# Kernel tuning notes

Measured on AMD Instinct MI355X. Metric: run time of the kernel, lower is better.

## Reference

```python
import jax, jax.numpy as jnp
import numpy as np

N_NODES = 100000
N_EDGES = 3200000
D_IN = 128
D_OUT = 128


def setup_inputs() -> dict:
    key = jax.random.key(0)
    k1, k2, k3, k4, k5, k6 = jax.random.split(key, 6)
    x = jax.random.normal(k1, (N_NODES, D_IN), dtype=jnp.float32)
    weight = jax.random.normal(k2, (D_OUT, D_IN), dtype=jnp.float32)
    bias = jax.random.normal(k3, (D_OUT,), dtype=jnp.float32)
    edge_vals = jax.random.uniform(k4, (N_EDGES,), dtype=jnp.float32)
    edge_rows = jax.random.randint(k5, (N_EDGES,), 0, N_NODES, dtype=jnp.int32)
    edge_cols = jax.random.randint(k6, (N_EDGES,), 0, N_NODES, dtype=jnp.int32)
    return {"x": x, "weight": weight, "bias": bias,
            "edge_vals": edge_vals, "edge_rows": edge_rows, "edge_cols": edge_cols}


def reference(x, weight, bias, edge_vals, edge_rows, edge_cols):
    # h = Linear(x): [N, D_OUT]
    h = jnp.einsum('ni,oi->no', x, weight) + bias
    # out = A @ h with A in COO form: out[r] += v * h[c]
    msgs = edge_vals[:, None] * h[edge_cols]  # [E, D_OUT]
    out = jax.ops.segment_sum(msgs, edge_rows, num_segments=N_NODES)
    return out
```

## Files before the change

### kernel.cpp

```cpp
#include <hip/hip_runtime.h>
#include <hip/hip_bf16.h>

#define D 128
#define RPB 256
#define RPB_SHIFT 8
#define NBMAX 512
#define P1CHUNK 8192
#define CAP 9216
#define OVFCAP 4096

using bf16x8 = __attribute__((ext_vector_type(8))) short;
using f32x4  = __attribute__((ext_vector_type(4))) float;
using f32x2  = __attribute__((ext_vector_type(2))) float;

static __device__ inline unsigned short f2bf(float f) {
    __hip_bfloat16 b = __float2bfloat16(f);
    return reinterpret_cast<unsigned short&>(b);
}

__global__ __launch_bounds__(256) void gemm_mfma_kernel(
    const float* __restrict__ x, const float* __restrict__ W,
    const float* __restrict__ bias, __hip_bfloat16* __restrict__ h, int N)
{
    __shared__ unsigned short sA[128 * 128];
    __shared__ unsigned short sB[128 * 128];

    const int tid   = threadIdx.x;
    const int nbase = blockIdx.x * 128;

#pragma unroll
    for (int it = 0; it < 16; ++it) {
        const int r = it * 8 + (tid >> 5);
        const int c = (tid & 31) * 4;
        const unsigned addr = (unsigned)((r * 256 + c * 2) ^ ((r & 7) << 4));

        const int gr = nbase + r;
        float4 xv = make_float4(0.f, 0.f, 0.f, 0.f);
        if (gr < N) xv = *reinterpret_cast<const float4*>(x + (size_t)gr * D + c);
        ushort4 xb = make_ushort4(f2bf(xv.x), f2bf(xv.y), f2bf(xv.z), f2bf(xv.w));
        *reinterpret_cast<ushort4*>(reinterpret_cast<char*>(sA) + addr) = xb;

        float4 wv = *reinterpret_cast<const float4*>(W + (size_t)r * D + c);
        ushort4 wb = make_ushort4(f2bf(wv.x), f2bf(wv.y), f2bf(wv.z), f2bf(wv.w));
        *reinterpret_cast<ushort4*>(reinterpret_cast<char*>(sB) + addr) = wb;
    }
    __syncthreads();

    const int wid  = tid >> 6;
    const int lane = tid & 63;
    const int wr   = (wid >> 1) * 64;
    const int wc   = (wid & 1) * 64;
    const int lrow = lane & 15;
    const int lkb  = (lane >> 4) * 16;

    f32x4 acc[4][4] = {};

#pragma unroll
    for (int kk = 0; kk < 4; ++kk) {
        const int kbyte = kk * 64 + lkb;
        bf16x8 a[4], b[4];
#pragma unroll
        for (int m = 0; m < 4; ++m) {
            const int row = wr + m * 16 + lrow;
            const unsigned addr = (unsigned)((row * 256 + kbyte) ^ ((row & 7) << 4));
            a[m] = *reinterpret_cast<const bf16x8*>(reinterpret_cast<const char*>(sA) + addr);
        }
#pragma unroll
        for (int n = 0; n < 4; ++n) {
            const int row = wc + n * 16 + lrow;
            const unsigned addr = (unsigned)((row * 256 + kbyte) ^ ((row & 7) << 4));
            b[n] = *reinterpret_cast<const bf16x8*>(reinterpret_cast<const char*>(sB) + addr);
        }
#pragma unroll
        for (int m = 0; m < 4; ++m)
#pragma unroll
            for (int n = 0; n < 4; ++n)
                acc[m][n] = __builtin_amdgcn_mfma_f32_16x16x32_bf16(a[m], b[n], acc[m][n], 0, 0, 0);
    }

    float bv[4];
#pragma unroll
    for (int n = 0; n < 4; ++n) bv[n] = bias[wc + n * 16 + lrow];

#pragma unroll
    for (int m = 0; m < 4; ++m) {
        const int row0 = nbase + wr + m * 16 + (lane >> 4) * 4;
#pragma unroll
        for (int n = 0; n < 4; ++n) {
            const int col = wc + n * 16 + lrow;
#pragma unroll
            for (int r = 0; r < 4; ++r) {
                const int grow = row0 + r;
                if (grow < N)
                    h[(size_t)grow * D + col] = __float2bfloat16(acc[m][n][r] + bv[n]);
            }
        }
    }
}

__global__ __launch_bounds__(256) void pass1_fixed_kernel(
    const int* __restrict__ rows, const int* __restrict__ cols,
    const float* __restrict__ vals,
    int* __restrict__ bcount,
    uint2* __restrict__ pairs,
    uint4* __restrict__ ovf,
    int NB, int E)
{
    __shared__ int srows[P1CHUNK];
    __shared__ int lh[NBMAX];
    __shared__ int lbase[NBMAX];

    const int tid  = threadIdx.x;
    const int base = blockIdx.x * P1CHUNK;

    for (int i = tid; i < NBMAX; i += 256) lh[i] = 0;
    __syncthreads();

#pragma unroll 4
    for (int it = 0; it < P1CHUNK / 256; ++it) {
        int e = base + it * 256 + tid;
        int r = (e < E) ? rows[e] : -1;
        srows[it * 256 + tid] = r;
        if (r >= 0) atomicAdd(&lh[r >> RPB_SHIFT], 1);
    }
    __syncthreads();

    for (int i = tid; i < NBMAX; i += 256) {
        int c = lh[i];
        lbase[i] = c ? (i * CAP + atomicAdd(&bcount[i], c)) : 0;
        lh[i] = 0;
    }
    __syncthreads();

#pragma unroll 4
    for (int it = 0; it < P1CHUNK / 256; ++it) {
        int e = base + it * 256 + tid;
        int r = srows[it * 256 + tid];
        if (r < 0) continue;
        int b = r >> RPB_SHIFT;
        int lofs = atomicAdd(&lh[b], 1);
        int pos = lbase[b] + lofs;
        if (pos < (b + 1) * CAP) {
            unsigned packed = ((unsigned)(r & (RPB - 1)) << 17) | (unsigned)cols[e];
            pairs[pos] = make_uint2(packed, __float_as_uint(vals[e]));
        } else {
            int oi = atomicAdd(&bcount[NB], 1);
            if (oi < OVFCAP)
                ovf[oi] = make_uint4((unsigned)r, (unsigned)cols[e],
                                     __float_as_uint(vals[e]), 0u);
        }
    }
}

__global__ __launch_bounds__(256) void pass2_fixed_kernel(
    uint2* __restrict__ pairs, const int* __restrict__ bcount,
    int* __restrict__ rowstart, int* __restrict__ rowend, int N)
{
    __shared__ uint2 st[CAP];
    __shared__ int rh[RPB];
    __shared__ int sc[RPB];
    __shared__ int cur[RPB];

    const int b   = blockIdx.x;
    const int tid = threadIdx.x;
    const int start = b * CAP;
    int cnt = bcount[b];
    if (cnt > CAP) cnt = CAP;

    rh[tid] = 0;
    __syncthreads();

    for (int i = tid; i < cnt; i += 256) {
        uint2 p = pairs[start + i];
        st[i] = p;
        atomicAdd(&rh[p.x >> 17], 1);
    }
    __syncthreads();

    int myc = rh[tid];
    sc[tid] = myc;
    __syncthreads();
    for (int off = 1; off < 256; off <<= 1) {
        int t = (tid >= off) ? sc[tid - off] : 0;
        __syncthreads();
        sc[tid] += t;
        __syncthreads();
    }
    int excl = sc[tid] - myc;
    cur[tid] = start + excl;
    int grow = b * RPB + tid;
    if (grow < N) {
        rowstart[grow] = start + excl;
        rowend[grow]   = start + excl + myc;
    }
    __syncthreads();

    for (int i = tid; i < cnt; i += 256) {
        uint2 p = st[i];
        int r = (int)(p.x >> 17);
        int pos = atomicAdd(&cur[r], 1);
        pairs[pos] = make_uint2(p.x & 0x1FFFFu, p.y);
    }
}

__global__ __launch_bounds__(256) void row_gather2_kernel(
    const __hip_bfloat16* __restrict__ hbf, const uint2* __restrict__ pairs,
    const int* __restrict__ rowstart, const int* __restrict__ rowend,
    float* __restrict__ out, int N)
{
    int row  = (int)((blockIdx.x * (size_t)blockDim.x + threadIdx.x) >> 6);
    int lane = threadIdx.x & 63;
    if (row >= N) return;

    int start = rowstart[row];
    int end   = rowend[row];

    const char* hb = reinterpret_cast<const char*>(hbf);
    const unsigned lbyte = (unsigned)lane << 2;
    float ax = 0.f, ay = 0.f;

    for (int e0 = start; e0 < end; e0 += 64) {
        int pl = e0 + lane;
        if (pl >= end) pl = end - 1;
        uint2 p = pairs[pl];
        int pc = (int)p.x, pv = (int)p.y;
        int m = end - e0; if (m > 64) m = 64;

        int idx = 0;
        const int m16 = m & ~15;
        for (; idx < m16; idx += 16) {
            unsigned c[16], vb[16], hv[16];
#pragma unroll
            for (int u = 0; u < 16; ++u) {
                c[u]  = (unsigned)__builtin_amdgcn_readlane(pc, idx + u);
                vb[u] = (unsigned)__builtin_amdgcn_readlane(pv, idx + u);
            }
#pragma unroll
            for (int u = 0; u < 16; ++u)
                hv[u] = *reinterpret_cast<const unsigned*>(hb + (((size_t)c[u]) << 8) + lbyte);
#pragma unroll
            for (int u = 0; u < 16; ++u) {
                float v = __uint_as_float(vb[u]);
                ax += v * __uint_as_float(hv[u] << 16);
                ay += v * __uint_as_float(hv[u] & 0xffff0000u);
            }
        }
        const int m8 = m & ~7;
        for (; idx < m8; idx += 8) {
            unsigned c[8], vb[8], hv[8];
#pragma unroll
            for (int u = 0; u < 8; ++u) {
                c[u]  = (unsigned)__builtin_amdgcn_readlane(pc, idx + u);
                vb[u] = (unsigned)__builtin_amdgcn_readlane(pv, idx + u);
            }
#pragma unroll
            for (int u = 0; u < 8; ++u)
                hv[u] = *reinterpret_cast<const unsigned*>(hb + (((size_t)c[u]) << 8) + lbyte);
#pragma unroll
            for (int u = 0; u < 8; ++u) {
                float v = __uint_as_float(vb[u]);
                ax += v * __uint_as_float(hv[u] << 16);
                ay += v * __uint_as_float(hv[u] & 0xffff0000u);
            }
        }
        for (; idx < m; ++idx) {
            unsigned c  = (unsigned)__builtin_amdgcn_readlane(pc, idx);
            unsigned vb = (unsigned)__builtin_amdgcn_readlane(pv, idx);
            unsigned hv = *reinterpret_cast<const unsigned*>(hb + (((size_t)c) << 8) + lbyte);
            float v = __uint_as_float(vb);
            ax += v * __uint_as_float(hv << 16);
            ay += v * __uint_as_float(hv & 0xffff0000u);
        }
    }

    f32x2 r2 = { ax, ay };
    __builtin_nontemporal_store(r2, reinterpret_cast<f32x2*>(out + (size_t)row * D) + lane);
}

__global__ __launch_bounds__(256) void fixup_kernel(
    const uint4* __restrict__ ovf, const int* __restrict__ ovfcnt,
    const __hip_bfloat16* __restrict__ hbf, float* __restrict__ out, int N)
{
    int cnt = *ovfcnt;
    if (cnt > OVFCAP) cnt = OVFCAP;
    const int wid  = threadIdx.x >> 6;
    const int lane = threadIdx.x & 63;
    const unsigned short* hb = reinterpret_cast<const unsigned short*>(hbf);
    for (int i = wid; i < cnt; i += 4) {
        uint4 e = ovf[i];
        if ((int)e.x >= N) continue;
        unsigned hv = *reinterpret_cast<const unsigned*>(hb + (size_t)e.y * D + lane * 2);
        float v = __uint_as_float(e.z);
        atomicAdd(out + (size_t)e.x * D + lane * 2,     v * __uint_as_float(hv << 16));
        atomicAdd(out + (size_t)e.x * D + lane * 2 + 1, v * __uint_as_float(hv & 0xffff0000u));
    }
}


__global__ __launch_bounds__(256) void gemm_kernel(
    const float* __restrict__ x, const float* __restrict__ W,
    const float* __restrict__ bias, float* __restrict__ h, int N)
{
    __shared__ float sWt[D][D];
    __shared__ float sx[16][D];
    const int tid = threadIdx.x;
    for (int idx = tid; idx < D * D; idx += 256) {
        int o = idx >> 7, i = idx & (D - 1);
        sWt[i][o] = W[idx];
    }
    const int nbase = blockIdx.x * 16;
    for (int idx = tid; idx < 16 * D; idx += 256) {
        int r = idx >> 7, i = idx & (D - 1);
        int n = nbase + r;
        sx[r][i] = (n < N) ? x[(size_t)n * D + i] : 0.0f;
    }
    __syncthreads();
    const int c = tid & (D - 1);
    const int rg = tid >> 7;
    float acc[8];
#pragma unroll
    for (int k = 0; k < 8; ++k) acc[k] = 0.0f;
#pragma unroll 4
    for (int i = 0; i < D; ++i) {
        float w = sWt[i][c];
#pragma unroll
        for (int k = 0; k < 8; ++k) acc[k] += sx[rg * 8 + k][i] * w;
    }
    const float b = bias[c];
#pragma unroll
    for (int k = 0; k < 8; ++k) {
        int n = nbase + rg * 8 + k;
        if (n < N) h[(size_t)n * D + c] = acc[k] + b;
    }
}

__global__ __launch_bounds__(256) void scatter_kernel(
    const float* __restrict__ h, const float* __restrict__ vals,
    const int* __restrict__ rows, const int* __restrict__ cols,
    float* __restrict__ out, int E)
{
    const int wid  = (int)((blockIdx.x * (size_t)blockDim.x + threadIdx.x) >> 6);
    const int lane = threadIdx.x & 63;
    if (wid >= E) return;
    const int   r = rows[wid];
    const int   c = cols[wid];
    const float v = vals[wid];
    float2 hv = *reinterpret_cast<const float2*>(h + (size_t)c * D + lane * 2);
    atomicAdd(out + (size_t)r * D + lane * 2,     v * hv.x);
    atomicAdd(out + (size_t)r * D + lane * 2 + 1, v * hv.y);
}

static inline size_t align16(size_t x) { return (x + 15) & ~(size_t)15; }

extern "C" void kernel_launch(void* const* d_in, const int* in_sizes, int n_in,
                              void* d_out, int out_size, void* d_ws, size_t ws_size,
                              hipStream_t stream)
{
    const float* x    = (const float*)d_in[0];
    const float* W    = (const float*)d_in[1];
    const float* bias = (const float*)d_in[2];
    const float* vals = (const float*)d_in[3];
    const int*   rows = (const int*)d_in[4];
    const int*   cols = (const int*)d_in[5];

    const int N = in_sizes[0] / D;
    const int E = in_sizes[3];
    float* out = (float*)d_out;

    const int NB = (N + RPB - 1) / RPB;
    const int GB = (N + 127) / 128;
    const int HB = (E + P1CHUNK - 1) / P1CHUNK;

    size_t f_h      = 0;
    size_t f_pairs  = f_h      + align16((size_t)N * D * 2);
    size_t f_rs     = f_pairs  + align16((size_t)NB * CAP * 8);
    size_t f_re     = f_rs     + align16((size_t)N * 4);
    size_t f_bcount = f_re     + align16((size_t)N * 4);
    size_t f_ovf    = f_bcount + align16((size_t)(NB + 1) * 4);
    size_t need_fast = f_ovf   + align16((size_t)OVFCAP * 16);

    if (ws_size >= need_fast && NB <= NBMAX && N <= (1 << 17)) {
        char* ws = (char*)d_ws;
        __hip_bfloat16* hbf = (__hip_bfloat16*)(ws + f_h);
        uint2* pairs        = (uint2*)(ws + f_pairs);
        int*   rowstart     = (int*)(ws + f_rs);
        int*   rowend       = (int*)(ws + f_re);
        int*   bcount       = (int*)(ws + f_bcount);
        uint4* ovf          = (uint4*)(ws + f_ovf);

        hipMemsetAsync(bcount, 0, (size_t)(NB + 1) * 4, stream);

        gemm_mfma_kernel<<<GB, 256, 0, stream>>>(x, W, bias, hbf, N);

        pass1_fixed_kernel<<<HB, 256, 0, stream>>>(
            rows, cols, vals, bcount, pairs, ovf, NB, E);

        pass2_fixed_kernel<<<NB, 256, 0, stream>>>(pairs, bcount, rowstart, rowend, N);

        int gblocks = (int)(((size_t)N * 64 + 255) / 256);
        row_gather2_kernel<<<gblocks, 256, 0, stream>>>(hbf, pairs, rowstart, rowend, out, N);

        fixup_kernel<<<1, 256, 0, stream>>>(ovf, bcount + NB, hbf, out, N);
    } else {
        float* h = (float*)d_ws;
        hipMemsetAsync(out, 0, (size_t)out_size * sizeof(float), stream);
        gemm_kernel<<<(N + 15) / 16, 256, 0, stream>>>(x, W, bias, h, N);
        scatter_kernel<<<(E + 3) / 4, 256, 0, stream>>>(h, vals, rows, cols, out, E);
    }
}
```

Baseline: 212.2 us.

## Fuse GEMM and COO bucketing pass into one launch with smaller GEMM tiles

Merges the bf16 MFMA linear-layer kernel and the edge bucketing pass1 kernel into a single launch. The first GB blocks do the GEMM and the remaining blocks do bucketing, so the two independent phases can run concurrently and one launch is removed. The GEMM tile shrinks from 128 to 64 rows per block to fit a shared 48KB buffer and to give more blocks. Each GEMM block now re-reads and converts the full weight matrix for half as many rows, and the bucketing blocks also reserve 48KB of shared memory, which may reduce occupancy.

```diff
diff --git a/kernel.cpp b/kernel.cpp
--- a/kernel.cpp
+++ b/kernel.cpp
@@ -18,136 +18,138 @@
     return reinterpret_cast<unsigned short&>(b);
 }
 
-__global__ __launch_bounds__(256) void gemm_mfma_kernel(
+__global__ __launch_bounds__(256) void gemm_pass1_kernel(
     const float* __restrict__ x, const float* __restrict__ W,
-    const float* __restrict__ bias, __hip_bfloat16* __restrict__ h, int N)
-{
-    __shared__ unsigned short sA[128 * 128];
-    __shared__ unsigned short sB[128 * 128];
-
-    const int tid   = threadIdx.x;
-    const int nbase = blockIdx.x * 128;
-
-#pragma unroll
-    for (int it = 0; it < 16; ++it) {
-        const int r = it * 8 + (tid >> 5);
-        const int c = (tid & 31) * 4;
-        const unsigned addr = (unsigned)((r * 256 + c * 2) ^ ((r & 7) << 4));
-
-        const int gr = nbase + r;
-        float4 xv = make_float4(0.f, 0.f, 0.f, 0.f);
-        if (gr < N) xv = *reinterpret_cast<const float4*>(x + (size_t)gr * D + c);
-        ushort4 xb = make_ushort4(f2bf(xv.x), f2bf(xv.y), f2bf(xv.z), f2bf(xv.w));
-        *reinterpret_cast<ushort4*>(reinterpret_cast<char*>(sA) + addr) = xb;
-
-        float4 wv = *reinterpret_cast<const float4*>(W + (size_t)r * D + c);
-        ushort4 wb = make_ushort4(f2bf(wv.x), f2bf(wv.y), f2bf(wv.z), f2bf(wv.w));
-        *reinterpret_cast<ushort4*>(reinterpret_cast<char*>(sB) + addr) = wb;
-    }
-    __syncthreads();
-
-    const int wid  = tid >> 6;
-    const int lane = tid & 63;
-    const int wr   = (wid >> 1) * 64;
-    const int wc   = (wid & 1) * 64;
-    const int lrow = lane & 15;
-    const int lkb  = (lane >> 4) * 16;
-
-    f32x4 acc[4][4] = {};
-
-#pragma unroll
-    for (int kk = 0; kk < 4; ++kk) {
-        const int kbyte = kk * 64 + lkb;
-        bf16x8 a[4], b[4];
-#pragma unroll
-        for (int m = 0; m < 4; ++m) {
-            const int row = wr + m * 16 + lrow;
-            const unsigned addr = (unsigned)((row * 256 + kbyte) ^ ((row & 7) << 4));
-            a[m] = *reinterpret_cast<const bf16x8*>(reinterpret_cast<const char*>(sA) + addr);
-        }
-#pragma unroll
-        for (int n = 0; n < 4; ++n) {
-            const int row = wc + n * 16 + lrow;
-            const unsigned addr = (unsigned)((row * 256 + kbyte) ^ ((row & 7) << 4));
-            b[n] = *reinterpret_cast<const bf16x8*>(reinterpret_cast<const char*>(sB) + addr);
-        }
-#pragma unroll
-        for (int m = 0; m < 4; ++m)
-#pragma unroll
-            for (int n = 0; n < 4; ++n)
-                acc[m][n] = __builtin_amdgcn_mfma_f32_16x16x32_bf16(a[m], b[n], acc[m][n], 0, 0, 0);
-    }
-
-    float bv[4];
-#pragma unroll
-    for (int n = 0; n < 4; ++n) bv[n] = bias[wc + n * 16 + lrow];
-
-#pragma unroll
-    for (int m = 0; m < 4; ++m) {
-        const int row0 = nbase + wr + m * 16 + (lane >> 4) * 4;
-#pragma unroll
-        for (int n = 0; n < 4; ++n) {
-            const int col = wc + n * 16 + lrow;
-#pragma unroll
-            for (int r = 0; r < 4; ++r) {
-                const int grow = row0 + r;
-                if (grow < N)
-                    h[(size_t)grow * D + col] = __float2bfloat16(acc[m][n][r] + bv[n]);
-            }
-        }
-    }
-}
-
-__global__ __launch_bounds__(256) void pass1_fixed_kernel(
+    const float* __restrict__ bias, __hip_bfloat16* __restrict__ h, int N,
     const int* __restrict__ rows, const int* __restrict__ cols,
     const float* __restrict__ vals,
     int* __restrict__ bcount,
     uint2* __restrict__ pairs,
     uint4* __restrict__ ovf,
-    int NB, int E)
-{
-    __shared__ int srows[P1CHUNK];
-    __shared__ int lh[NBMAX];
-    __shared__ int lbase[NBMAX];
-
-    const int tid  = threadIdx.x;
-    const int base = blockIdx.x * P1CHUNK;
-
-    for (int i = tid; i < NBMAX; i += 256) lh[i] = 0;
-    __syncthreads();
+    int NB, int E, int GB)
+{
+    __shared__ __align__(16) char smem[48 * 1024];
+    const int tid = threadIdx.x;
+
+    if (blockIdx.x >= GB) {
+        int* srows = reinterpret_cast<int*>(smem);
+        int* lh    = reinterpret_cast<int*>(smem + 32 * 1024);
+        int* lbase = reinterpret_cast<int*>(smem + 34 * 1024);
+
+        const int base = (blockIdx.x - GB) * P1CHUNK;
+
+        for (int i = tid; i < NBMAX; i += 256) lh[i] = 0;
+        __syncthreads();
 
 #pragma unroll 4
-    for (int it = 0; it < P1CHUNK / 256; ++it) {
-        int e = base + it * 256 + tid;
-        int r = (e < E) ? rows[e] : -1;
-        srows[it * 256 + tid] = r;
-        if (r >= 0) atomicAdd(&lh[r >> RPB_SHIFT], 1);
-    }
-    __syncthreads();
-
-    for (int i = tid; i < NBMAX; i += 256) {
-        int c = lh[i];
-        lbase[i] = c ? (i * CAP + atomicAdd(&bcount[i], c)) : 0;
-        lh[i] = 0;
-    }
-    __syncthreads();
+        for (int it = 0; it < P1CHUNK / 256; ++it) {
+            int e = base + it * 256 + tid;
+            int r = (e < E) ? rows[e] : -1;
+            srows[it * 256 + tid] = r;
+            if (r >= 0) atomicAdd(&lh[r >> RPB_SHIFT], 1);
+        }
+        __syncthreads();
+
+        for (int i = tid; i < NBMAX; i += 256) {
+            int c = lh[i];
+            lbase[i] = c ? (i * CAP + atomicAdd(&bcount[i], c)) : 0;
+            lh[i] = 0;
+        }
+        __syncthreads();
 
 #pragma unroll 4
-    for (int it = 0; it < P1CHUNK / 256; ++it) {
-        int e = base + it * 256 + tid;
-        int r = srows[it * 256 + tid];
-        if (r < 0) continue;
-        int b = r >> RPB_SHIFT;
-        int lofs = atomicAdd(&lh[b], 1);
-        int pos = lbase[b] + lofs;
-        if (pos < (b + 1) * CAP) {
-            unsigned packed = ((unsigned)(r & (RPB - 1)) << 17) | (unsigned)cols[e];
-            pairs[pos] = make_uint2(packed, __float_as_uint(vals[e]));
-        } else {
-            int oi = atomicAdd(&bcount[NB], 1);
-            if (oi < OVFCAP)
-                ovf[oi] = make_uint4((unsigned)r, (unsigned)cols[e],
-                                     __float_as_uint(vals[e]), 0u);
+        for (int it = 0; it < P1CHUNK / 256; ++it) {
+            int e = base + it * 256 + tid;
+            int r = srows[it * 256 + tid];
+            if (r < 0) continue;
+            int b = r >> RPB_SHIFT;
+            int lofs = atomicAdd(&lh[b], 1);
+            int pos = lbase[b] + lofs;
+            if (pos < (b + 1) * CAP) {
+                unsigned packed = ((unsigned)(r & (RPB - 1)) << 17) | (unsigned)cols[e];
+                pairs[pos] = make_uint2(packed, __float_as_uint(vals[e]));
+            } else {
+                int oi = atomicAdd(&bcount[NB], 1);
+                if (oi < OVFCAP)
+                    ovf[oi] = make_uint4((unsigned)r, (unsigned)cols[e],
+                                         __float_as_uint(vals[e]), 0u);
+            }
+        }
+        return;
+    }
+
+    char* sA = smem;
+    char* sB = smem + 16 * 1024;
+    const int nbase = blockIdx.x * 64;
+
+#pragma unroll
+    for (int it = 0; it < 16; ++it) {
+        const int r = it * 8 + (tid >> 5);
+        const int c = (tid & 31) * 4;
+        const unsigned addr = (unsigned)((r * 256 + c * 2) ^ ((r & 7) << 4));
+
+        float4 wv = *reinterpret_cast<const float4*>(W + (size_t)r * D + c);
+        ushort4 wb = make_ushort4(f2bf(wv.x), f2bf(wv.y), f2bf(wv.z), f2bf(wv.w));
+        *reinterpret_cast<ushort4*>(sB + addr) = wb;
+
+        if (it < 8) {
+            const int gr = nbase + r;
+            float4 xv = make_float4(0.f, 0.f, 0.f, 0.f);
+            if (gr < N) xv = *reinterpret_cast<const float4*>(x + (size_t)gr * D + c);
+            ushort4 xb = make_ushort4(f2bf(xv.x), f2bf(xv.y), f2bf(xv.z), f2bf(xv.w));
+            *reinterpret_cast<ushort4*>(sA + addr) = xb;
+        }
+    }
+    __syncthreads();
+
+    const int wid  = tid >> 6;
+    const int lane = tid & 63;
+    const int wr   = (wid >> 1) * 32;
+    const int wc   = (wid & 1) * 64;
+    const int lrow = lane & 15;
+    const int lkb  = (lane >> 4) * 16;
+
+    f32x4 acc[2][4] = {};
+
+#pragma unroll
+    for (int kk = 0; kk < 4; ++kk) {
+        const int kbyte = kk * 64 + lkb;
+        bf16x8 a[2], b[4];
+#pragma unroll
+        for (int m = 0; m < 2; ++m) {
+            const int row = wr + m * 16 + lrow;
+            const unsigned addr = (unsigned)((row * 256 + kbyte) ^ ((row & 7) << 4));
+            a[m] = *reinterpret_cast<const bf16x8*>(sA + addr);
+        }
+#pragma unroll
+        for (int n = 0; n < 4; ++n) {
+            const int row = wc + n * 16 + lrow;
+            const unsigned addr = (unsigned)((row * 256 + kbyte) ^ ((row & 7) << 4));
+            b[n] = *reinterpret_cast<const bf16x8*>(sB + addr);
+        }
+#pragma unroll
+        for (int m = 0; m < 2; ++m)
+#pragma unroll
+            for (int n = 0; n < 4; ++n)
+                acc[m][n] = __builtin_amdgcn_mfma_f32_16x16x32_bf16(a[m], b[n], acc[m][n], 0, 0, 0);
+    }
+
+    float bv[4];
+#pragma unroll
+    for (int n = 0; n < 4; ++n) bv[n] = bias[wc + n * 16 + lrow];
+
+#pragma unroll
+    for (int m = 0; m < 2; ++m) {
+        const int row0 = nbase + wr + m * 16 + (lane >> 4) * 4;
+#pragma unroll
+        for (int n = 0; n < 4; ++n) {
+            const int col = wc + n * 16 + lrow;
+#pragma unroll
+            for (int r = 0; r < 4; ++r) {
+                const int grow = row0 + r;
+                if (grow < N)
+                    h[(size_t)grow * D + col] = __float2bfloat16(acc[m][n][r] + bv[n]);
+            }
         }
     }
 }
@@ -368,7 +370,7 @@
     float* out = (float*)d_out;
 
     const int NB = (N + RPB - 1) / RPB;
-    const int GB = (N + 127) / 128;
+    const int GB = (N + 63) / 64;
     const int HB = (E + P1CHUNK - 1) / P1CHUNK;
 
     size_t f_h      = 0;
@@ -390,10 +392,8 @@
 
         hipMemsetAsync(bcount, 0, (size_t)(NB + 1) * 4, stream);
 
-        gemm_mfma_kernel<<<GB, 256, 0, stream>>>(x, W, bias, hbf, N);
-
-        pass1_fixed_kernel<<<HB, 256, 0, stream>>>(
-            rows, cols, vals, bcount, pairs, ovf, NB, E);
+        gemm_pass1_kernel<<<GB + HB, 256, 0, stream>>>(
+            x, W, bias, hbf, N, rows, cols, vals, bcount, pairs, ovf, NB, E, GB);
 
         pass2_fixed_kernel<<<NB, 256, 0, stream>>>(pairs, bcount, rowstart, rowend, N);
 
```

New measurement: 201.4 us. 5.1% less time.
